# Kernel optimization log

Hardware: AMD Instinct MI355X
Metric: run time of the kernel (lower is better)

## Reference

```python
import jax, jax.numpy as jnp
import numpy as np
import math

S, B, E, H = 2048, 2, 1024, 16
D = E // H
LN_EPS = 1e-5


def setup_inputs() -> dict:
    key = jax.random.key(0)
    ks = jax.random.split(key, 8)
    src = jax.random.normal(ks[0], (S, B, E), dtype=jnp.float32)
    # causal attention mask: 1 = attend, 0 = masked
    src_mask = jnp.tril(jnp.ones((S, S), dtype=jnp.int32))
    in_proj_w = jax.random.normal(ks[1], (2 * E, E), dtype=jnp.float32) * 0.02
    in_proj_b = jnp.zeros((2 * E,), dtype=jnp.float32)
    out_proj_w = jax.random.normal(ks[2], (E, E), dtype=jnp.float32) * 0.02
    out_proj_b = jnp.zeros((E,), dtype=jnp.float32)
    ln_g = jnp.ones((E,), dtype=jnp.float32)
    ln_b = jnp.zeros((E,), dtype=jnp.float32)
    return {"src": src, "src_mask": src_mask, "in_proj_w": in_proj_w,
            "in_proj_b": in_proj_b, "out_proj_w": out_proj_w,
            "out_proj_b": out_proj_b, "ln_g": ln_g, "ln_b": ln_b}


def _layernorm(x, g, b):
    mu = jnp.mean(x, axis=-1, keepdims=True)
    var = jnp.mean(jnp.square(x - mu), axis=-1, keepdims=True)
    return (x - mu) * jax.lax.rsqrt(var + LN_EPS) * g + b


def reference(src, src_mask, in_proj_w, in_proj_b, out_proj_w, out_proj_b, ln_g, ln_b):
    # src: (S, B, E)
    x_norm = _layernorm(src, ln_g, ln_b)
    proj = jax.nn.silu(x_norm @ in_proj_w.T + in_proj_b)     # (S, B, 2E)
    qkv, u = jnp.split(proj, 2, axis=-1)                     # each (S, B, E)
    qkv = qkv.reshape(S, B, H, D)                            # q = k = v = qkv
    # scores: (B, H, S_q, S_k)
    scores = jnp.einsum('sbhd,tbhd->bhst', qkv, qkv) / math.sqrt(D)
    # torch does masked_fill(-inf) then silu; silu(-inf) -> 0 in the limit,
    # which is the intended semantics (masked positions contribute nothing).
    weights = jnp.where(src_mask[None, None, :, :] == 0, 0.0, jax.nn.silu(scores))
    # attn_dropout is identity at eval
    attn = jnp.einsum('bhst,tbhd->sbhd', weights, qkv).reshape(S, B, E)
    gated = attn * u
    out = src + (gated @ out_proj_w.T + out_proj_b)          # out_dropout = identity
    return out
```

## Files before the change

### kernel.cpp

```cpp
#include <hip/hip_runtime.h>


typedef __attribute__((ext_vector_type(8))) short  short8;
typedef __attribute__((ext_vector_type(4))) float  floatx4;
typedef __attribute__((ext_vector_type(4))) float  fvec4;
typedef __attribute__((ext_vector_type(4))) unsigned short usvec4;

__device__ __forceinline__ unsigned short f2b(float f) {
  unsigned u = __builtin_bit_cast(unsigned, f);
  u += 0x7FFFu + ((u >> 16) & 1u);
  return (unsigned short)(u >> 16);
}
__device__ __forceinline__ float b2f(unsigned short h) {
  unsigned u = ((unsigned)h) << 16;
  return __builtin_bit_cast(float, u);
}
__device__ __forceinline__ float silu_f(float x) {
  return __fdividef(x, 1.f + __expf(-x));
}
__device__ __forceinline__ void async_copy16(void* lds, const void* g) {
  __builtin_amdgcn_global_load_lds(
      (__attribute__((address_space(1))) void*)(g),
      (__attribute__((address_space(3))) void*)(lds), 16, 0, 0);
}

__global__ void cvt_bf16(const float* __restrict__ s, unsigned short* __restrict__ d, int n4) {
  int i = blockIdx.x * 256 + threadIdx.x;
  if (i < n4) {
    fvec4 v = ((const fvec4*)s)[i];
    usvec4 o = { f2b(v.x), f2b(v.y), f2b(v.z), f2b(v.w) };
    ((usvec4*)d)[i] = o;
  }
}

__global__ __launch_bounds__(256) void ln_kernel(
    const float* __restrict__ x, const float* __restrict__ g,
    const float* __restrict__ b, unsigned short* __restrict__ xn) {
  const int row = blockIdx.x, t = threadIdx.x;
  const float* xr = x + (long)row * 1024;
  fvec4 v = ((const fvec4*)xr)[t];
  float s  = v.x + v.y + v.z + v.w;
  float s2 = v.x*v.x + v.y*v.y + v.z*v.z + v.w*v.w;
  #pragma unroll
  for (int off = 32; off; off >>= 1) { s += __shfl_down(s, off); s2 += __shfl_down(s2, off); }
  __shared__ float red[8];
  int lane = t & 63, w = t >> 6;
  if (lane == 0) { red[w] = s; red[4 + w] = s2; }
  __syncthreads();
  s  = red[0] + red[1] + red[2] + red[3];
  s2 = red[4] + red[5] + red[6] + red[7];
  float mu  = s * (1.f / 1024.f);
  float var = s2 * (1.f / 1024.f) - mu * mu;
  float rs  = rsqrtf(var + 1e-5f);
  fvec4 gg = ((const fvec4*)g)[t];
  fvec4 bb = ((const fvec4*)b)[t];
  usvec4 o = { f2b((v.x - mu) * rs * gg.x + bb.x),
               f2b((v.y - mu) * rs * gg.y + bb.y),
               f2b((v.z - mu) * rs * gg.z + bb.z),
               f2b((v.w - mu) * rs * gg.w + bb.w) };
  ((usvec4*)(xn + (long)row * 1024))[t] = o;
}

template <int EPI>
__global__ __launch_bounds__(256, 2) void gemm_bt(
    const unsigned short* __restrict__ A, const unsigned short* __restrict__ Bw,
    const float* __restrict__ bias, const float* __restrict__ src,
    unsigned short* __restrict__ out0, unsigned short* __restrict__ out1,
    float* __restrict__ outf, int N, int K) {
  __shared__ __align__(16) unsigned short sA[128 * 32];
  __shared__ __align__(16) unsigned short sB[128 * 32];
  const int t = threadIdx.x;
  const int lane = t & 63, l15 = lane & 15, quad = lane >> 4;
  const int w = t >> 6, wm = w >> 1, wn = w & 1;
  const int m0 = blockIdx.y * 128, n0 = blockIdx.x * 128;

  floatx4 acc[4][4];
  const floatx4 z4 = {0.f, 0.f, 0.f, 0.f};
  #pragma unroll
  for (int i = 0; i < 4; i++)
    #pragma unroll
    for (int j = 0; j < 4; j++) acc[i][j] = z4;

  const int nk = K >> 5;
  for (int kt = 0; kt < nk; ++kt) {
    const int k0 = kt << 5;
    __syncthreads();
    #pragma unroll
    for (int c = 0; c < 2; ++c) {
      int slot = c * 256 + t;
      int row = slot >> 2, col = (slot & 3) << 3;
      async_copy16(&sA[slot * 8], &A[(m0 + row) * K + k0 + col]);
      async_copy16(&sB[slot * 8], &Bw[(n0 + row) * K + k0 + col]);
    }
    __syncthreads();
    short8 af[4], bf[4];
    #pragma unroll
    for (int mr = 0; mr < 4; mr++)
      af[mr] = *(const short8*)&sA[(wm * 64 + mr * 16 + l15) * 32 + quad * 8];
    #pragma unroll
    for (int nr = 0; nr < 4; nr++)
      bf[nr] = *(const short8*)&sB[(wn * 64 + nr * 16 + l15) * 32 + quad * 8];
    #pragma unroll
    for (int mr = 0; mr < 4; mr++)
      #pragma unroll
      for (int nr = 0; nr < 4; nr++)
        acc[mr][nr] = __builtin_amdgcn_mfma_f32_16x16x32_bf16(af[mr], bf[nr], acc[mr][nr], 0, 0, 0);
  }

  #pragma unroll
  for (int mr = 0; mr < 4; mr++) {
    int gm0 = m0 + wm * 64 + mr * 16 + quad * 4;
    #pragma unroll
    for (int nr = 0; nr < 4; nr++) {
      int gn = n0 + wn * 64 + nr * 16 + l15;
      float bv = bias[gn];
      if (EPI == 0) {
        unsigned short* dst = (gn < 1024) ? (out0 + gn) : (out1 + gn - 1024);
        #pragma unroll
        for (int r = 0; r < 4; r++) {
          float v = acc[mr][nr][r] + bv;
          dst[(long)(gm0 + r) * 1024] = f2b(silu_f(v));
        }
      } else {
        #pragma unroll
        for (int r = 0; r < 4; r++) {
          long idx = (long)(gm0 + r) * N + gn;
          outf[idx] = acc[mr][nr][r] + bv + src[idx];
        }
      }
    }
  }
}

#define SKS 72
#define SVS 136
#define SPS 136
__global__ __launch_bounds__(256, 4) void attn_kernel(
    const unsigned short* __restrict__ qkv, const unsigned short* __restrict__ u,
    unsigned short* __restrict__ gated) {
  __shared__ __align__(16) unsigned char smem[128 * SKS * 2 + 64 * SVS * 2];
  unsigned short* sK  = (unsigned short*)smem;
  unsigned short* sP  = (unsigned short*)smem;
  unsigned short* sVt = (unsigned short*)(smem + 128 * SKS * 2);

  const int t = threadIdx.x, lane = t & 63, l15 = lane & 15, quad = lane >> 4;
  const int w = t >> 6;
  const int gg = blockIdx.x >> 5, sub = gg >> 3, g = gg & 7;
  const int qi = (sub == 0) ? g : (sub == 1) ? (31 - g) : (sub == 2) ? (g + 8) : (23 - g);
  const int bh = blockIdx.x & 31;
  const int b = bh >> 4, h = bh & 15;
  const long base = (long)b * 1024 + h * 64;
  const int q0 = qi * 64;
  const int rg = t >> 3, dg = t & 7;

  #pragma unroll
  for (int c = 0; c < 2; ++c) {
    int slot = c * 256 + t, row = slot >> 3, cg = slot & 7;
    *(short8*)&sK[row * SKS + cg * 8] =
        *(const short8*)&qkv[base + (long)(q0 + row) * 2048 + cg * 8];
  }
  __syncthreads();
  short8 qf[4][2];
  #pragma unroll
  for (int mr = 0; mr < 4; mr++)
    #pragma unroll
    for (int ks = 0; ks < 2; ks++)
      qf[mr][ks] = *(const short8*)&sK[(mr * 16 + l15) * SKS + ks * 32 + quad * 8];

  floatx4 oacc[4];
  const floatx4 z4 = {0.f, 0.f, 0.f, 0.f};
  #pragma unroll
  for (int i = 0; i < 4; i++) oacc[i] = z4;

  const int nkt = (qi >> 1) + 1;
  for (int kt = 0; kt < nkt; ++kt) {
    const int t0 = kt * 128;
    __syncthreads();
    short8 kv[4];
    #pragma unroll
    for (int i = 0; i < 4; ++i)
      kv[i] = *(const short8*)&qkv[base + (long)(t0 + rg * 4 + i) * 2048 + dg * 8];
    #pragma unroll
    for (int i = 0; i < 4; ++i)
      *(short8*)&sK[(rg * 4 + i) * SKS + dg * 8] = kv[i];
    #pragma unroll
    for (int j = 0; j < 8; ++j) {
      unsigned lo = (unsigned)(unsigned short)kv[0][j] | ((unsigned)(unsigned short)kv[1][j] << 16);
      unsigned hi = (unsigned)(unsigned short)kv[2][j] | ((unsigned)(unsigned short)kv[3][j] << 16);
      unsigned long long v64 = (unsigned long long)lo | ((unsigned long long)hi << 32);
      *(unsigned long long*)&sVt[(dg * 8 + j) * SVS + rg * 4] = v64;
    }
    __syncthreads();
    floatx4 sacc[4][2];
    #pragma unroll
    for (int i = 0; i < 4; i++) { sacc[i][0] = z4; sacc[i][1] = z4; }
    #pragma unroll
    for (int ks = 0; ks < 2; ++ks) {
      short8 kf[2];
      #pragma unroll
      for (int nr = 0; nr < 2; nr++)
        kf[nr] = *(const short8*)&sK[(w * 32 + nr * 16 + l15) * SKS + ks * 32 + quad * 8];
      #pragma unroll
      for (int mr = 0; mr < 4; mr++)
        #pragma unroll
        for (int nr = 0; nr < 2; nr++)
          sacc[mr][nr] = __builtin_amdgcn_mfma_f32_16x16x32_bf16(qf[mr][ks], kf[nr], sacc[mr][nr], 0, 0, 0);
    }
    const bool diag = (kt == nkt - 1);
    #pragma unroll
    for (int mr = 0; mr < 4; mr++) {
      int row0 = mr * 16 + quad * 4;
      #pragma unroll
      for (int nr = 0; nr < 2; nr++) {
        int col = w * 32 + nr * 16 + l15;
        #pragma unroll
        for (int r = 0; r < 4; r++) {
          float v = silu_f(sacc[mr][nr][r] * 0.125f);
          if (diag && (q0 + row0 + r < t0 + col)) v = 0.f;
          sacc[mr][nr][r] = v;
        }
      }
    }
    __syncthreads();
    #pragma unroll
    for (int mr = 0; mr < 4; mr++)
      #pragma unroll
      for (int nr = 0; nr < 2; nr++)
        #pragma unroll
        for (int r = 0; r < 4; r++)
          sP[(mr * 16 + quad * 4 + r) * SPS + w * 32 + nr * 16 + l15] = f2b(sacc[mr][nr][r]);
    __syncthreads();
    #pragma unroll
    for (int ts = 0; ts < 4; ++ts) {
      short8 vfr = *(const short8*)&sVt[(w * 16 + l15) * SVS + ts * 32 + quad * 8];
      #pragma unroll
      for (int mr = 0; mr < 4; mr++) {
        short8 pf = *(const short8*)&sP[(mr * 16 + l15) * SPS + ts * 32 + quad * 8];
        oacc[mr] = __builtin_amdgcn_mfma_f32_16x16x32_bf16(pf, vfr, oacc[mr], 0, 0, 0);
      }
    }
  }
  #pragma unroll
  for (int mr = 0; mr < 4; mr++)
    #pragma unroll
    for (int r = 0; r < 4; r++) {
      int s = q0 + mr * 16 + quad * 4 + r;
      long addr = (long)s * 2048 + base + w * 16 + l15;
      gated[addr] = f2b(oacc[mr][r] * b2f(u[addr]));
    }
}

extern "C" void kernel_launch(void* const* d_in, const int* in_sizes, int n_in,
                              void* d_out, int out_size, void* d_ws, size_t ws_size,
                              hipStream_t stream) {
  const float* src = (const float*)d_in[0];
  const float* w1  = (const float*)d_in[2];
  const float* b1  = (const float*)d_in[3];
  const float* w2  = (const float*)d_in[4];
  const float* b2  = (const float*)d_in[5];
  const float* lng = (const float*)d_in[6];
  const float* lnb = (const float*)d_in[7];
  float* out = (float*)d_out;

  char* ws = (char*)d_ws;
  unsigned short* xn    = (unsigned short*)(ws + 0);
  unsigned short* qkv   = (unsigned short*)(ws + 8388608);
  unsigned short* uu    = (unsigned short*)(ws + 16777216);
  unsigned short* gated = (unsigned short*)(ws + 25165824);
  unsigned short* w1b   = (unsigned short*)(ws + 33554432);
  unsigned short* w2b   = (unsigned short*)(ws + 37748736);

  cvt_bf16<<<2048, 256, 0, stream>>>(w1, w1b, 524288);
  cvt_bf16<<<1024, 256, 0, stream>>>(w2, w2b, 262144);
  ln_kernel<<<4096, 256, 0, stream>>>(src, lng, lnb, xn);
  gemm_bt<0><<<dim3(16, 32), 256, 0, stream>>>(xn, w1b, b1, nullptr, qkv, uu, nullptr, 2048, 1024);
  attn_kernel<<<1024, 256, 0, stream>>>(qkv, uu, gated);
  gemm_bt<1><<<dim3(8, 32), 256, 0, stream>>>(gated, w2b, b2, src, nullptr, nullptr, out, 1024, 1024);
}
```

Baseline: 218.8 us.

## Split GEMM kernels, retile output GEMM, swizzle V transpose, cheaper SiLU

The templated GEMM is split into specialized input and output kernels. The output GEMM uses 128x64 tiles so it launches 512 blocks instead of 256 and fills more CUs. The attention V-transpose now uses byte-perm instructions and an XOR-style swizzled LDS layout to cut bank conflicts on the transposed writes and reads. SiLU switches to exp2 plus a hardware reciprocal, which trades a little accuracy for fewer instructions.

```diff
diff --git a/kernel.cpp b/kernel.cpp
--- a/kernel.cpp
+++ b/kernel.cpp
@@ -5,6 +5,7 @@
 typedef __attribute__((ext_vector_type(4))) float  floatx4;
 typedef __attribute__((ext_vector_type(4))) float  fvec4;
 typedef __attribute__((ext_vector_type(4))) unsigned short usvec4;
+typedef __attribute__((ext_vector_type(4))) int    intx4;
 
 __device__ __forceinline__ unsigned short f2b(float f) {
   unsigned u = __builtin_bit_cast(unsigned, f);
@@ -16,7 +17,8 @@
   return __builtin_bit_cast(float, u);
 }
 __device__ __forceinline__ float silu_f(float x) {
-  return __fdividef(x, 1.f + __expf(-x));
+  float e = __builtin_amdgcn_exp2f(-1.44269504f * x);
+  return x * __builtin_amdgcn_rcpf(1.f + e);
 }
 __device__ __forceinline__ void async_copy16(void* lds, const void* g) {
   __builtin_amdgcn_global_load_lds(
@@ -61,18 +63,17 @@
   ((usvec4*)(xn + (long)row * 1024))[t] = o;
 }
 
-template <int EPI>
-__global__ __launch_bounds__(256, 2) void gemm_bt(
+__global__ __launch_bounds__(256, 2) void gemm_in(
     const unsigned short* __restrict__ A, const unsigned short* __restrict__ Bw,
-    const float* __restrict__ bias, const float* __restrict__ src,
-    unsigned short* __restrict__ out0, unsigned short* __restrict__ out1,
-    float* __restrict__ outf, int N, int K) {
+    const float* __restrict__ bias,
+    unsigned short* __restrict__ out0, unsigned short* __restrict__ out1) {
   __shared__ __align__(16) unsigned short sA[128 * 32];
   __shared__ __align__(16) unsigned short sB[128 * 32];
   const int t = threadIdx.x;
   const int lane = t & 63, l15 = lane & 15, quad = lane >> 4;
   const int w = t >> 6, wm = w >> 1, wn = w & 1;
   const int m0 = blockIdx.y * 128, n0 = blockIdx.x * 128;
+  const int K = 1024;
 
   floatx4 acc[4][4];
   const floatx4 z4 = {0.f, 0.f, 0.f, 0.f};
@@ -81,8 +82,7 @@
     #pragma unroll
     for (int j = 0; j < 4; j++) acc[i][j] = z4;
 
-  const int nk = K >> 5;
-  for (int kt = 0; kt < nk; ++kt) {
+  for (int kt = 0; kt < 32; ++kt) {
     const int k0 = kt << 5;
     __syncthreads();
     #pragma unroll
@@ -114,19 +114,71 @@
     for (int nr = 0; nr < 4; nr++) {
       int gn = n0 + wn * 64 + nr * 16 + l15;
       float bv = bias[gn];
-      if (EPI == 0) {
-        unsigned short* dst = (gn < 1024) ? (out0 + gn) : (out1 + gn - 1024);
-        #pragma unroll
-        for (int r = 0; r < 4; r++) {
-          float v = acc[mr][nr][r] + bv;
-          dst[(long)(gm0 + r) * 1024] = f2b(silu_f(v));
-        }
-      } else {
-        #pragma unroll
-        for (int r = 0; r < 4; r++) {
-          long idx = (long)(gm0 + r) * N + gn;
-          outf[idx] = acc[mr][nr][r] + bv + src[idx];
-        }
+      unsigned short* dst = (gn < 1024) ? (out0 + gn) : (out1 + gn - 1024);
+      #pragma unroll
+      for (int r = 0; r < 4; r++) {
+        float v = acc[mr][nr][r] + bv;
+        dst[(long)(gm0 + r) * 1024] = f2b(silu_f(v));
+      }
+    }
+  }
+}
+
+__global__ __launch_bounds__(256, 2) void gemm_out(
+    const unsigned short* __restrict__ A, const unsigned short* __restrict__ Bw,
+    const float* __restrict__ bias, const float* __restrict__ src,
+    float* __restrict__ outf) {
+  __shared__ __align__(16) unsigned short sA[128 * 32];
+  __shared__ __align__(16) unsigned short sB[64 * 32];
+  const int t = threadIdx.x;
+  const int lane = t & 63, l15 = lane & 15, quad = lane >> 4;
+  const int w = t >> 6;
+  const int m0 = blockIdx.y * 128, n0 = blockIdx.x * 64;
+
+  floatx4 acc[2][4];
+  const floatx4 z4 = {0.f, 0.f, 0.f, 0.f};
+  #pragma unroll
+  for (int i = 0; i < 2; i++)
+    #pragma unroll
+    for (int j = 0; j < 4; j++) acc[i][j] = z4;
+
+  for (int kt = 0; kt < 32; ++kt) {
+    const int k0 = kt << 5;
+    __syncthreads();
+    #pragma unroll
+    for (int c = 0; c < 2; ++c) {
+      int slot = c * 256 + t;
+      int row = slot >> 2, col = (slot & 3) << 3;
+      async_copy16(&sA[slot * 8], &A[(m0 + row) * 1024 + k0 + col]);
+    }
+    { int row = t >> 2, col = (t & 3) << 3;
+      async_copy16(&sB[t * 8], &Bw[(n0 + row) * 1024 + k0 + col]); }
+    __syncthreads();
+    short8 af[2], bf[4];
+    #pragma unroll
+    for (int mr = 0; mr < 2; mr++)
+      af[mr] = *(const short8*)&sA[(w * 32 + mr * 16 + l15) * 32 + quad * 8];
+    #pragma unroll
+    for (int nr = 0; nr < 4; nr++)
+      bf[nr] = *(const short8*)&sB[(nr * 16 + l15) * 32 + quad * 8];
+    #pragma unroll
+    for (int mr = 0; mr < 2; mr++)
+      #pragma unroll
+      for (int nr = 0; nr < 4; nr++)
+        acc[mr][nr] = __builtin_amdgcn_mfma_f32_16x16x32_bf16(af[mr], bf[nr], acc[mr][nr], 0, 0, 0);
+  }
+
+  #pragma unroll
+  for (int mr = 0; mr < 2; mr++) {
+    int gm0 = m0 + w * 32 + mr * 16 + quad * 4;
+    #pragma unroll
+    for (int nr = 0; nr < 4; nr++) {
+      int gn = n0 + nr * 16 + l15;
+      float bv = bias[gn];
+      #pragma unroll
+      for (int r = 0; r < 4; r++) {
+        long idx = (long)(gm0 + r) * 1024 + gn;
+        outf[idx] = acc[mr][nr][r] + bv + src[idx];
       }
     }
   }
@@ -152,6 +204,7 @@
   const long base = (long)b * 1024 + h * 64;
   const int q0 = qi * 64;
   const int rg = t >> 3, dg = t & 7;
+  const int swz0 = (rg >> 1) + dg;
 
   #pragma unroll
   for (int c = 0; c < 2; ++c) {
@@ -172,6 +225,9 @@
   #pragma unroll
   for (int i = 0; i < 4; i++) oacc[i] = z4;
 
+  const int d_rd = w * 16 + l15;
+  const int rsw0 = quad + (d_rd & 7) + (d_rd >> 3);
+
   const int nkt = (qi >> 1) + 1;
   for (int kt = 0; kt < nkt; ++kt) {
     const int t0 = kt * 128;
@@ -183,12 +239,26 @@
     #pragma unroll
     for (int i = 0; i < 4; ++i)
       *(short8*)&sK[(rg * 4 + i) * SKS + dg * 8] = kv[i];
-    #pragma unroll
-    for (int j = 0; j < 8; ++j) {
-      unsigned lo = (unsigned)(unsigned short)kv[0][j] | ((unsigned)(unsigned short)kv[1][j] << 16);
-      unsigned hi = (unsigned)(unsigned short)kv[2][j] | ((unsigned)(unsigned short)kv[3][j] << 16);
-      unsigned long long v64 = (unsigned long long)lo | ((unsigned long long)hi << 32);
-      *(unsigned long long*)&sVt[(dg * 8 + j) * SVS + rg * 4] = v64;
+    {
+      intx4 k0 = __builtin_bit_cast(intx4, kv[0]);
+      intx4 k1 = __builtin_bit_cast(intx4, kv[1]);
+      intx4 k2 = __builtin_bit_cast(intx4, kv[2]);
+      intx4 k3 = __builtin_bit_cast(intx4, kv[3]);
+      #pragma unroll
+      for (int jj = 0; jj < 4; ++jj) {
+        unsigned lo = __builtin_amdgcn_perm((unsigned)k1[jj], (unsigned)k0[jj], 0x05040100u);
+        unsigned hi = __builtin_amdgcn_perm((unsigned)k3[jj], (unsigned)k2[jj], 0x05040100u);
+        int j = 2 * jj, d = dg * 8 + j;
+        int gsw = (swz0 + j) & 15;
+        *(unsigned long long*)&sVt[d * SVS + gsw * 8 + (rg & 1) * 4] =
+            (unsigned long long)lo | ((unsigned long long)hi << 32);
+        lo = __builtin_amdgcn_perm((unsigned)k1[jj], (unsigned)k0[jj], 0x07060302u);
+        hi = __builtin_amdgcn_perm((unsigned)k3[jj], (unsigned)k2[jj], 0x07060302u);
+        j = 2 * jj + 1; d = dg * 8 + j;
+        gsw = (swz0 + j) & 15;
+        *(unsigned long long*)&sVt[d * SVS + gsw * 8 + (rg & 1) * 4] =
+            (unsigned long long)lo | ((unsigned long long)hi << 32);
+      }
     }
     __syncthreads();
     floatx4 sacc[4][2];
@@ -232,7 +302,8 @@
     __syncthreads();
     #pragma unroll
     for (int ts = 0; ts < 4; ++ts) {
-      short8 vfr = *(const short8*)&sVt[(w * 16 + l15) * SVS + ts * 32 + quad * 8];
+      int gsw = (ts * 4 + rsw0) & 15;
+      short8 vfr = *(const short8*)&sVt[d_rd * SVS + gsw * 8];
       #pragma unroll
       for (int mr = 0; mr < 4; mr++) {
         short8 pf = *(const short8*)&sP[(mr * 16 + l15) * SPS + ts * 32 + quad * 8];
@@ -273,7 +344,7 @@
   cvt_bf16<<<2048, 256, 0, stream>>>(w1, w1b, 524288);
   cvt_bf16<<<1024, 256, 0, stream>>>(w2, w2b, 262144);
   ln_kernel<<<4096, 256, 0, stream>>>(src, lng, lnb, xn);
-  gemm_bt<0><<<dim3(16, 32), 256, 0, stream>>>(xn, w1b, b1, nullptr, qkv, uu, nullptr, 2048, 1024);
+  gemm_in<<<dim3(16, 32), 256, 0, stream>>>(xn, w1b, b1, qkv, uu);
   attn_kernel<<<1024, 256, 0, stream>>>(qkv, uu, gated);
-  gemm_bt<1><<<dim3(8, 32), 256, 0, stream>>>(gated, w2b, b2, src, nullptr, nullptr, out, 1024, 1024);
-}
+  gemm_out<<<dim3(16, 32), 256, 0, stream>>>(gated, w2b, b2, src, out);
+}
```

Result: faster. 193.2 us (-11.7%).
